# Optimization experiments

Measured on AMD Instinct MI355X. Metric: run time of the kernel, lower is better.

The kernel has to match this reference:

```python
import jax, jax.numpy as jnp
import numpy as np

N, F, T, H, E, OUT, HEADS = 20000, 32, 12, 64, 320000, 12, 2


def setup_inputs() -> dict:
    key = jax.random.key(0)
    ks = iter(jax.random.split(key, 40))

    def nrm(shape, scale):
        return jax.random.normal(next(ks), shape, jnp.float32) * scale

    g0 = 2 * H + F   # gate input dim, cell 0
    g1 = 2 * H + H   # gate input dim, cell 1
    inp = {
        "x": nrm((N, F, T), 1.0),
        "edge_index": jax.random.randint(next(ks), (2, E), 0, N, dtype=jnp.int32),
        "edge_attr": jax.random.uniform(next(ks), (E, 2), dtype=jnp.float32),
        # cell 0: GCNConv + GRU gates (weights stored [in, out])
        "Wg0": nrm((F, H), F ** -0.5), "bg0": nrm((H,), 0.02),
        "Wu0": nrm((g0, H), g0 ** -0.5), "bu0": nrm((H,), 0.02),
        "Wr0": nrm((g0, H), g0 ** -0.5), "br0": nrm((H,), 0.02),
        "Wc0": nrm((g0, H), g0 ** -0.5), "bc0": nrm((H,), 0.02),
        # cell 1
        "Wg1": nrm((H, H), H ** -0.5), "bg1": nrm((H,), 0.02),
        "Wu1": nrm((g1, H), g1 ** -0.5), "bu1": nrm((H,), 0.02),
        "Wr1": nrm((g1, H), g1 ** -0.5), "br1": nrm((H,), 0.02),
        "Wc1": nrm((g1, H), g1 ** -0.5), "bc1": nrm((H,), 0.02),
        # temporal multi-head attention (torch layout: [out, in])
        "in_proj_w": nrm((3 * H, H), H ** -0.5), "in_proj_b": nrm((3 * H,), 0.02),
        "out_proj_w": nrm((H, H), H ** -0.5), "out_proj_b": nrm((H,), 0.02),
        # output head ([in, out])
        "out_w": nrm((H, OUT), H ** -0.5), "out_b": nrm((OUT,), 0.02),
    }
    return inp


def reference(x, edge_index, edge_attr,
              Wg0, bg0, Wu0, bu0, Wr0, br0, Wc0, bc0,
              Wg1, bg1, Wu1, bu1, Wr1, br1, Wc1, bc1,
              in_proj_w, in_proj_b, out_proj_w, out_proj_b,
              out_w, out_b):
    n, f, t = x.shape
    h_dim = Wg0.shape[1]
    src, dst = edge_index[0], edge_index[1]
    w = edge_attr[:, -1]

    # GCN normalization with self-loops (PyG gcn_norm)
    loop = jnp.arange(n)
    src_all = jnp.concatenate([src, loop])
    dst_all = jnp.concatenate([dst, loop])
    w_all = jnp.concatenate([w, jnp.ones((n,), x.dtype)])
    deg = jax.ops.segment_sum(w_all, dst_all, num_segments=n)
    dinv = jnp.where(deg > 0, jax.lax.rsqrt(deg), 0.0)
    norm = dinv[src_all] * w_all * dinv[dst_all]  # [E+N]

    def gcn(xi, W, b):
        xw = xi @ W  # [N, H]
        msg = norm[:, None] * xw[src_all]  # gather from sources
        return jax.ops.segment_sum(msg, dst_all, num_segments=n) + b

    def cell(xi, h, W, b, Wu, bu, Wr, br, Wc, bc):
        g = jax.nn.sigmoid(gcn(xi, W, b))
        zu = jnp.concatenate([xi, g, h], axis=-1)
        u = jax.nn.sigmoid(zu @ Wu + bu)
        r = jax.nn.sigmoid(zu @ Wr + br)
        zc = jnp.concatenate([xi, g, r * h], axis=-1)
        c = jnp.tanh(zc @ Wc + bc)
        return u * h + (1.0 - u) * c

    def step(carry, x_t):
        h0, h1 = carry
        h0 = cell(x_t, h0, Wg0, bg0, Wu0, bu0, Wr0, br0, Wc0, bc0)
        h1 = cell(h0, h1, Wg1, bg1, Wu1, bu1, Wr1, br1, Wc1, bc1)
        return (h0, h1), h1

    x_seq = jnp.transpose(x, (2, 0, 1))  # [T, N, F]
    h0 = jnp.zeros((n, h_dim), x.dtype)
    _, h_seq = jax.lax.scan(step, (h0, h0), x_seq)  # [T, N, H] (== [S, B, H])

    # temporal multi-head self-attention per node
    heads = HEADS
    dh = h_dim // heads
    qkv = h_seq @ in_proj_w.T + in_proj_b  # [T, N, 3H]
    q, k, v = jnp.split(qkv, 3, axis=-1)

    def split_heads(a):
        return jnp.transpose(a.reshape(t, n, heads, dh), (1, 2, 0, 3))  # [N, h, T, dh]

    q, k, v = split_heads(q), split_heads(k), split_heads(v)
    scores = jnp.einsum('nhtd,nhsd->nhts', q, k) / jnp.sqrt(jnp.asarray(dh, x.dtype))
    attn = jax.nn.softmax(scores, axis=-1)
    o = jnp.einsum('nhts,nhsd->nhtd', attn, v)
    o = jnp.transpose(o, (2, 0, 1, 3)).reshape(t, n, h_dim)
    o = o @ out_proj_w.T + out_proj_b  # [T, N, H]

    h_attn = o.mean(axis=0)  # agg='mean' over sequence -> [N, H]
    return h_attn @ out_w + out_b  # [N, OUT]
```

## Files before the change

kernel.cpp:

```cpp
#include <hip/hip_runtime.h>
#include <math.h>

#define NN 20000
#define FF 32
#define TT 12
#define HH 64
#define EE 320000
#define OUTD 12
#define CB1 1250
#define GB  2500

typedef __attribute__((ext_vector_type(8))) short short8;
typedef __attribute__((ext_vector_type(4))) float floatx4;

__device__ __forceinline__ float aexp2(float x) {
    float r; asm("v_exp_f32 %0, %1" : "=v"(r) : "v"(x)); return r;
}
__device__ __forceinline__ float arcp(float x) {
    float r; asm("v_rcp_f32 %0, %1" : "=v"(r) : "v"(x)); return r;
}
#define LOG2E 1.44269504088896f
__device__ __forceinline__ float fsig(float x) { return arcp(1.f + aexp2(-LOG2E * x)); }
__device__ __forceinline__ float ftanh(float x) {
    return fmaf(-2.f, arcp(1.f + aexp2(2.f * LOG2E * x)), 1.f);
}

__device__ __forceinline__ unsigned short bf16rne(float f) {
    union { float f; unsigned u; } v; v.f = f;
    unsigned u = v.u;
    u += 0x7fffu + ((u >> 16) & 1u);
    return (unsigned short)(u >> 16);
}
__device__ __forceinline__ float lof(unsigned v) {
    union { unsigned u; float f; } x; x.u = v << 16; return x.f;
}
__device__ __forceinline__ float hif(unsigned v) {
    union { unsigned u; float f; } x; x.u = v & 0xffff0000u; return x.f;
}
__device__ __forceinline__ unsigned packbf(float a, float b) {
    return (unsigned)bf16rne(a) | ((unsigned)bf16rne(b) << 16);
}

#define MFMA(a, b, c) __builtin_amdgcn_mfma_f32_16x16x32_bf16((a), (b), (c), 0, 0, 0)


__global__ void init_all(float* deg, int* cnt, float* h0f1, float* h1f1,
                         unsigned* h0s2u, unsigned* h1s0u) {
    int i = blockIdx.x * 256 + threadIdx.x;
    if (i < NN) { deg[i] = 1.0f; cnt[i] = 0; }
    if (i < NN * HH) { h0f1[i] = 0.f; h1f1[i] = 0.f; }
    if (i < NN * HH / 2) { h0s2u[i] = 0u; h1s0u[i] = 0u; }
}

__global__ void edge_accum_kernel(const int* ei, const float* ea, float* deg, int* cnt) {
    int e = blockIdx.x * 256 + threadIdx.x;
    if (e >= EE) return;
    int d = ei[EE + e];
    float w = ea[e * 2 + 1];
    atomicAdd(&deg[d], w);
    atomicAdd(&cnt[d], 1);
}

__global__ void scan_dinv(const int* cnt, int* rowptr, int* cursor,
                          const float* deg, float* dinv) {
    if (blockIdx.x != 0) {
        int i = (blockIdx.x - 1) * 1024 + threadIdx.x;
        if (i < NN) dinv[i] = rsqrtf(deg[i]);
        return;
    }
    __shared__ int wsum[16];
    int tid = threadIdx.x;
    int lane = tid & 63, w = tid >> 6;
    int run = 0;
    for (int base = 0; base < NN; base += 1024) {
        int idx = base + tid;
        int c = (idx < NN) ? cnt[idx] : 0;
        int v = c;
        #pragma unroll
        for (int off = 1; off < 64; off <<= 1) {
            int t = __shfl_up(v, off, 64);
            if (lane >= off) v += t;
        }
        if (lane == 63) wsum[w] = v;
        __syncthreads();
        if (tid < 16) {
            int x = wsum[tid];
            #pragma unroll
            for (int off = 1; off < 16; off <<= 1) {
                int t = __shfl_up(x, off, 64);
                if (tid >= off) x += t;
            }
            wsum[tid] = x;
        }
        __syncthreads();
        int waveoff = (w > 0) ? wsum[w - 1] : 0;
        int excl = run + waveoff + (v - c);
        if (idx < NN) { rowptr[idx] = excl; cursor[idx] = excl; }
        run += wsum[15];
        __syncthreads();
    }
    if (tid == 0) rowptr[NN] = run;
}

__global__ void fill_kernel(const int* ei, const float* ea, const float* dinv,
                            int* cursor, int2* colval) {
    int e = blockIdx.x * 256 + threadIdx.x;
    if (e >= EE) return;
    int s = ei[e], d = ei[EE + e];
    float w = ea[e * 2 + 1];
    int pos = atomicAdd(&cursor[d], 1);
    colval[pos] = make_int2(s, __float_as_int(dinv[s] * w * dinv[d]));
}

#define TPB 1250
#define WCB 336
__global__ void prep_misc(const float* __restrict__ x, unsigned short* __restrict__ xTs,
                          const float* Wg0, const float* Wu0, const float* Wr0, const float* Wc0,
                          const float* Wg1, const float* Wu1, const float* Wr1, const float* Wc1,
                          const float* ipw,
                          short* Wg0T, short* Wu0T, short* Wr0T, short* Wc0T,
                          short* Wg1T, short* Wu1T, short* Wr1T, short* Wc1T, short* ipwB,
                          const float* opw, const float* opb, const float* ow, const float* ob,
                          float* OW2, float* ob2) {
    int b = blockIdx.x;
    if (b < TPB) {
        __shared__ float tl[16 * 416];
        int n0 = b * 16;
        const float* xb = x + (size_t)n0 * 384;
        int tid = threadIdx.x;
        #pragma unroll
        for (int k = 0; k < 24; ++k) {
            int i = tid + 256 * k;
            float v = xb[i];
            int nn = i / 384;
            int rem = i - nn * 384;
            int f = rem / 12;
            int t2 = rem - f * 12;
            tl[nn * 416 + f * 13 + t2] = v;
        }
        __syncthreads();
        #pragma unroll
        for (int k = 0; k < 24; ++k) {
            int o = tid + 256 * k;
            int f = o & 31;
            int nn = (o >> 5) & 15;
            int t = o >> 9;
            xTs[(size_t)t * (NN * FF) + (size_t)(n0 + nn) * 32 + f] =
                bf16rne(tl[nn * 416 + f * 13 + t]);
        }
        return;
    }
    if (b < TPB + WCB) {
        int i = (b - TPB) * 256 + threadIdx.x;
        if (i < 2048) { int n = i / 32, k = i % 32; Wg0T[i] = (short)bf16rne(Wg0[k * 64 + n]); return; }
        i -= 2048;
        if (i < 10240) { int n = i / 160, k = i % 160; Wu0T[i] = (short)bf16rne(Wu0[k * 64 + n]); return; }
        i -= 10240;
        if (i < 10240) { int n = i / 160, k = i % 160; Wr0T[i] = (short)bf16rne(Wr0[k * 64 + n]); return; }
        i -= 10240;
        if (i < 10240) { int n = i / 160, k = i % 160; Wc0T[i] = (short)bf16rne(Wc0[k * 64 + n]); return; }
        i -= 10240;
        if (i < 4096) { int n = i / 64, k = i % 64; Wg1T[i] = (short)bf16rne(Wg1[k * 64 + n]); return; }
        i -= 4096;
        if (i < 12288) { int n = i / 192, k = i % 192; Wu1T[i] = (short)bf16rne(Wu1[k * 64 + n]); return; }
        i -= 12288;
        if (i < 12288) { int n = i / 192, k = i % 192; Wr1T[i] = (short)bf16rne(Wr1[k * 64 + n]); return; }
        i -= 12288;
        if (i < 12288) { int n = i / 192, k = i % 192; Wc1T[i] = (short)bf16rne(Wc1[k * 64 + n]); return; }
        i -= 12288;
        if (i < 12288) { ipwB[i] = (short)bf16rne(ipw[i]); }
        return;
    }
    {
        int i = (b - TPB - WCB) * 256 + threadIdx.x;
        if (i < 64 * OUTD) {
            int k = i / OUTD, d = i - k * OUTD;
            float acc = 0.f;
            for (int j = 0; j < 64; ++j) acc += opw[j * 64 + k] * ow[j * OUTD + d];
            OW2[i] = acc;
        } else if (i < 64 * OUTD + OUTD) {
            int d = i - 64 * OUTD;
            float acc = ob[d];
            for (int j = 0; j < 64; ++j) acc += opb[j] * ow[j * OUTD + d];
            ob2[d] = acc;
        }
    }
}

__global__ void gather_raw32(const unsigned short* __restrict__ xTs, const float* __restrict__ dinv,
                             const int* __restrict__ rowptr, const int2* __restrict__ colval,
                             unsigned short* __restrict__ aggxs) {
    const unsigned* src = (const unsigned*)(xTs + (size_t)blockIdx.y * NN * 32);
    unsigned* dst = (unsigned*)(aggxs + (size_t)blockIdx.y * NN * 32);
    int node = blockIdx.x * 16 + (threadIdx.x >> 4);
    int l2 = threadIdx.x & 15;
    float di = dinv[node];
    float dd = di * di;
    unsigned v = src[node * 16 + l2];
    float a0 = dd * lof(v), a1 = dd * hif(v);
    int s = rowptr[node], e = rowptr[node + 1];
    int j = s;
    for (; j + 3 < e; j += 4) {
        int2 cv0 = colval[j], cv1 = colval[j + 1], cv2 = colval[j + 2], cv3 = colval[j + 3];
        float w0 = __int_as_float(cv0.y), w1 = __int_as_float(cv1.y);
        float w2 = __int_as_float(cv2.y), w3 = __int_as_float(cv3.y);
        unsigned v0 = src[cv0.x * 16 + l2], v1 = src[cv1.x * 16 + l2];
        unsigned v2 = src[cv2.x * 16 + l2], v3 = src[cv3.x * 16 + l2];
        a0 += w0 * lof(v0) + w1 * lof(v1) + w2 * lof(v2) + w3 * lof(v3);
        a1 += w0 * hif(v0) + w1 * hif(v1) + w2 * hif(v2) + w3 * hif(v3);
    }
    for (; j < e; ++j) {
        int2 cv = colval[j];
        unsigned vv = src[cv.x * 16 + l2];
        float w = __int_as_float(cv.y);
        a0 += w * lof(vv); a1 += w * hif(vv);
    }
    dst[node * 16 + l2] = packbf(a0, a1);
}

__device__ __forceinline__ void gather_g1_body(
    int blk, const unsigned short* __restrict__ y0s, const float* __restrict__ dinv,
    const int* __restrict__ rowptr, const int2* __restrict__ colval,
    const float* __restrict__ bg1, unsigned short* __restrict__ g1s) {
    const unsigned* yp = (const unsigned*)y0s;
    int node = blk * 8 + (threadIdx.x >> 5);
    int l2 = threadIdx.x & 31;
    float di = dinv[node];
    float dd = di * di;
    unsigned v = yp[node * 32 + l2];
    float a0 = dd * lof(v), a1 = dd * hif(v);
    int s = rowptr[node], e = rowptr[node + 1];
    int j = s;
    for (; j + 3 < e; j += 4) {
        int2 cv0 = colval[j], cv1 = colval[j + 1], cv2 = colval[j + 2], cv3 = colval[j + 3];
        float w0 = __int_as_float(cv0.y), w1 = __int_as_float(cv1.y);
        float w2 = __int_as_float(cv2.y), w3 = __int_as_float(cv3.y);
        unsigned v0 = yp[cv0.x * 32 + l2], v1 = yp[cv1.x * 32 + l2];
        unsigned v2 = yp[cv2.x * 32 + l2], v3 = yp[cv3.x * 32 + l2];
        a0 += w0 * lof(v0) + w1 * lof(v1) + w2 * lof(v2) + w3 * lof(v3);
        a1 += w0 * hif(v0) + w1 * hif(v1) + w2 * hif(v2) + w3 * hif(v3);
    }
    for (; j < e; ++j) {
        int2 cv = colval[j];
        unsigned vv = yp[cv.x * 32 + l2];
        float w = __int_as_float(cv.y);
        a0 += w * lof(vv); a1 += w * hif(vv);
    }
    float g0v = fsig(a0 + bg1[2 * l2]);
    float g1v = fsig(a1 + bg1[2 * l2 + 1]);
    ((unsigned*)g1s)[node * 32 + l2] = packbf(g0v, g1v);
}


__launch_bounds__(256, 4)
__global__ void mfma_g0(const unsigned short* __restrict__ aggxs, const short* __restrict__ Wg0T,
                        const float* __restrict__ bg0, unsigned short* __restrict__ g0s) {
    int tid = threadIdx.x;
    int wv = tid >> 6, lane = tid & 63;
    int quad = lane >> 4, ln = lane & 15;
    int m0 = blockIdx.x * 64 + wv * 16;
    short8 af = *reinterpret_cast<const short8*>(aggxs + (size_t)(m0 + ln) * 32 + quad * 8);
    floatx4 z = {0.f, 0.f, 0.f, 0.f};
    floatx4 acc[4] = {z, z, z, z};
    #pragma unroll
    for (int ct = 0; ct < 4; ++ct) {
        short8 bf = *reinterpret_cast<const short8*>(Wg0T + (size_t)(ct * 16 + ln) * 32 + quad * 8);
        acc[ct] = MFMA(af, bf, acc[ct]);
    }
    #pragma unroll
    for (int ct = 0; ct < 4; ++ct) {
        int col = ct * 16 + ln;
        float bb = bg0[col];
        #pragma unroll
        for (int r = 0; r < 4; ++r) {
            int row = m0 + quad * 4 + r;
            g0s[(size_t)row * 64 + col] = bf16rne(fsig(acc[ct][r] + bb));
        }
    }
}


__device__ __forceinline__ void cell0_body(
    int m0, short* T,
    const unsigned short* __restrict__ xt, const unsigned short* __restrict__ g0,
    const float* __restrict__ h0f, const unsigned short* __restrict__ h0s,
    const short* __restrict__ Wu0T, const short* __restrict__ Wr0T,
    const short* __restrict__ Wc0T, const short* __restrict__ Wg1T,
    const float* __restrict__ bu0, const float* __restrict__ br0,
    const float* __restrict__ bc0,
    float* __restrict__ h0nf, unsigned short* __restrict__ h0ns,
    unsigned short* __restrict__ y0s) {
    int tid = threadIdx.x;
    int wv = tid >> 6, lane = tid & 63;
    int quad = lane >> 4, ln = lane & 15;
    int arow = m0 + ln;
    int col = wv * 16 + ln;

    short8 af[5];
    af[0] = *reinterpret_cast<const short8*>(xt + (size_t)arow * 32 + quad * 8);
    af[1] = *reinterpret_cast<const short8*>(g0 + (size_t)arow * 64 + quad * 8);
    af[2] = *reinterpret_cast<const short8*>(g0 + (size_t)arow * 64 + 32 + quad * 8);
    af[3] = *reinterpret_cast<const short8*>(h0s + (size_t)arow * 64 + quad * 8);
    af[4] = *reinterpret_cast<const short8*>(h0s + (size_t)arow * 64 + 32 + quad * 8);

    floatx4 z = {0.f, 0.f, 0.f, 0.f};
    floatx4 aU = z, aR = z;
    const short* bu = Wu0T + (size_t)col * 160;
    const short* br = Wr0T + (size_t)col * 160;
    #pragma unroll
    for (int kc = 0; kc < 5; ++kc) {
        int ko = kc * 32 + quad * 8;
        aU = MFMA(af[kc], *reinterpret_cast<const short8*>(bu + ko), aU);
        aR = MFMA(af[kc], *reinterpret_cast<const short8*>(br + ko), aR);
    }
    float bU = bu0[col], bR = br0[col];
    float uu[4], hv[4];
    #pragma unroll
    for (int r = 0; r < 4; ++r) {
        int grow = m0 + quad * 4 + r;
        uu[r] = fsig(aU[r] + bU);
        hv[r] = h0f[(size_t)grow * 64 + col];
        float rh = fsig(aR[r] + bR) * hv[r];
        T[(quad * 4 + r) * 72 + col] = (short)bf16rne(rh);
    }
    __syncthreads();

    short8 ar0 = *reinterpret_cast<const short8*>(T + ln * 72 + quad * 8);
    short8 ar1 = *reinterpret_cast<const short8*>(T + ln * 72 + 32 + quad * 8);
    floatx4 aC = z;
    const short* bc = Wc0T + (size_t)col * 160;
    #pragma unroll
    for (int kc = 0; kc < 3; ++kc)
        aC = MFMA(af[kc], *reinterpret_cast<const short8*>(bc + kc * 32 + quad * 8), aC);
    aC = MFMA(ar0, *reinterpret_cast<const short8*>(bc + 96 + quad * 8), aC);
    aC = MFMA(ar1, *reinterpret_cast<const short8*>(bc + 128 + quad * 8), aC);
    __syncthreads();

    float bC = bc0[col];
    #pragma unroll
    for (int r = 0; r < 4; ++r) {
        int grow = m0 + quad * 4 + r;
        float cv = ftanh(aC[r] + bC);
        float hn = uu[r] * hv[r] + (1.f - uu[r]) * cv;
        unsigned short hb = bf16rne(hn);
        h0nf[(size_t)grow * 64 + col] = hn;
        h0ns[(size_t)grow * 64 + col] = hb;
        T[(quad * 4 + r) * 72 + col] = (short)hb;
    }
    __syncthreads();

    short8 ah0 = *reinterpret_cast<const short8*>(T + ln * 72 + quad * 8);
    short8 ah1 = *reinterpret_cast<const short8*>(T + ln * 72 + 32 + quad * 8);
    floatx4 aY = z;
    const short* bg = Wg1T + (size_t)col * 64;
    aY = MFMA(ah0, *reinterpret_cast<const short8*>(bg + quad * 8), aY);
    aY = MFMA(ah1, *reinterpret_cast<const short8*>(bg + 32 + quad * 8), aY);
    #pragma unroll
    for (int r = 0; r < 4; ++r) {
        int grow = m0 + quad * 4 + r;
        y0s[(size_t)grow * 64 + col] = bf16rne(aY[r]);
    }
}

__device__ __forceinline__ void cell1_body(
    int m0, short* T,
    const unsigned short* __restrict__ h0s, const unsigned short* __restrict__ g1s,
    const float* __restrict__ h1f, const unsigned short* __restrict__ h1s,
    const short* __restrict__ Wu1T, const short* __restrict__ Wr1T,
    const short* __restrict__ Wc1T,
    const float* __restrict__ bu1, const float* __restrict__ br1,
    const float* __restrict__ bc1,
    float* __restrict__ h1nf, unsigned short* __restrict__ h1ns) {
    int tid = threadIdx.x;
    int wv = tid >> 6, lane = tid & 63;
    int quad = lane >> 4, ln = lane & 15;
    int arow = m0 + ln;
    int col = wv * 16 + ln;

    short8 af[6];
    af[0] = *reinterpret_cast<const short8*>(h0s + (size_t)arow * 64 + quad * 8);
    af[1] = *reinterpret_cast<const short8*>(h0s + (size_t)arow * 64 + 32 + quad * 8);
    af[2] = *reinterpret_cast<const short8*>(g1s + (size_t)arow * 64 + quad * 8);
    af[3] = *reinterpret_cast<const short8*>(g1s + (size_t)arow * 64 + 32 + quad * 8);
    af[4] = *reinterpret_cast<const short8*>(h1s + (size_t)arow * 64 + quad * 8);
    af[5] = *reinterpret_cast<const short8*>(h1s + (size_t)arow * 64 + 32 + quad * 8);

    floatx4 z = {0.f, 0.f, 0.f, 0.f};
    floatx4 aU = z, aR = z;
    const short* bu = Wu1T + (size_t)col * 192;
    const short* br = Wr1T + (size_t)col * 192;
    #pragma unroll
    for (int kc = 0; kc < 6; ++kc) {
        int ko = kc * 32 + quad * 8;
        aU = MFMA(af[kc], *reinterpret_cast<const short8*>(bu + ko), aU);
        aR = MFMA(af[kc], *reinterpret_cast<const short8*>(br + ko), aR);
    }
    float bU = bu1[col], bR = br1[col];
    float uu[4], hv[4];
    #pragma unroll
    for (int r = 0; r < 4; ++r) {
        int grow = m0 + quad * 4 + r;
        uu[r] = fsig(aU[r] + bU);
        hv[r] = h1f[(size_t)grow * 64 + col];
        float rh = fsig(aR[r] + bR) * hv[r];
        T[(quad * 4 + r) * 72 + col] = (short)bf16rne(rh);
    }
    __syncthreads();

    short8 ar0 = *reinterpret_cast<const short8*>(T + ln * 72 + quad * 8);
    short8 ar1 = *reinterpret_cast<const short8*>(T + ln * 72 + 32 + quad * 8);
    floatx4 aC = z;
    const short* bc = Wc1T + (size_t)col * 192;
    #pragma unroll
    for (int kc = 0; kc < 4; ++kc)
        aC = MFMA(af[kc], *reinterpret_cast<const short8*>(bc + kc * 32 + quad * 8), aC);
    aC = MFMA(ar0, *reinterpret_cast<const short8*>(bc + 128 + quad * 8), aC);
    aC = MFMA(ar1, *reinterpret_cast<const short8*>(bc + 160 + quad * 8), aC);

    float bC = bc1[col];
    #pragma unroll
    for (int r = 0; r < 4; ++r) {
        int grow = m0 + quad * 4 + r;
        float cv = ftanh(aC[r] + bC);
        float hn = uu[r] * hv[r] + (1.f - uu[r]) * cv;
        h1nf[(size_t)grow * 64 + col] = hn;
        h1ns[(size_t)grow * 64 + col] = bf16rne(hn);
    }
}


struct PipeArgs {
    const float* dinv; const int* rowptr; const int2* colval;
    const short* Wu0T; const short* Wr0T; const short* Wc0T; const short* Wg1T;
    const float* bu0; const float* br0; const float* bc0;
    const short* Wu1T; const short* Wr1T; const short* Wc1T;
    const float* bu1; const float* br1; const float* bc1; const float* bg1;
    int c0n;
    const unsigned short* c0_xt; const unsigned short* c0_g0;
    const float* c0_hf_in; const unsigned short* c0_hs_in;
    float* c0_hf_out; unsigned short* c0_hs_out; unsigned short* c0_y0_out;
    int gn;
    const unsigned short* g_y0; unsigned short* g_g1;
    int c1n;
    const unsigned short* c1_h0s; const unsigned short* c1_g1;
    const float* c1_hf_in; const unsigned short* c1_hs_in;
    float* c1_hf_out; unsigned short* c1_hs_out;
};

__launch_bounds__(256, 6)
__global__ void pipe_step(PipeArgs A) {
    __shared__ short T[16 * 72];
    int b = blockIdx.x;
    if (b < A.c0n) {
        cell0_body(b * 16, T, A.c0_xt, A.c0_g0, A.c0_hf_in, A.c0_hs_in,
                   A.Wu0T, A.Wr0T, A.Wc0T, A.Wg1T, A.bu0, A.br0, A.bc0,
                   A.c0_hf_out, A.c0_hs_out, A.c0_y0_out);
        return;
    }
    b -= A.c0n;
    if (b < A.gn) {
        gather_g1_body(b, A.g_y0, A.dinv, A.rowptr, A.colval, A.bg1, A.g_g1);
        return;
    }
    b -= A.gn;
    cell1_body(b * 16, T, A.c1_h0s, A.c1_g1, A.c1_hf_in, A.c1_hs_in,
               A.Wu1T, A.Wr1T, A.Wc1T, A.bu1, A.br1, A.bc1,
               A.c1_hf_out, A.c1_hs_out);
}

__launch_bounds__(256, 5)
__global__ void attn_fused(const unsigned short* __restrict__ hseqs,
                           const short* __restrict__ ipwB, const float* __restrict__ ipb,
                           const float* __restrict__ OW2, const float* __restrict__ ob2,
                           float* __restrict__ out) {
    __shared__ unsigned short qtile[4][16 * 200];
    __shared__ float fbuf[4][64];
    __shared__ float wbuf[4][32];
    int wv = threadIdx.x >> 6, lane = threadIdx.x & 63;
    int node = blockIdx.x * 4 + wv;
    int quad = lane >> 4, ln = lane & 15;
    unsigned short* q = qtile[wv];
    float* sob = fbuf[wv];
    float* W = wbuf[wv];

    short8 zero8 = {0, 0, 0, 0, 0, 0, 0, 0};
    short8 af0 = zero8, af1 = zero8;
    if (ln < TT) {
        const unsigned short* hp = hseqs + ((size_t)ln * NN + node) * 64;
        af0 = *reinterpret_cast<const short8*>(hp + quad * 8);
        af1 = *reinterpret_cast<const short8*>(hp + 32 + quad * 8);
    }
    floatx4 z = {0.f, 0.f, 0.f, 0.f};
    #pragma unroll
    for (int ct = 0; ct < 12; ++ct) {
        const short* br = ipwB + (size_t)(ct * 16 + ln) * 64;
        floatx4 acc = MFMA(af0, *reinterpret_cast<const short8*>(br + quad * 8), z);
        acc = MFMA(af1, *reinterpret_cast<const short8*>(br + 32 + quad * 8), acc);
        int col = ct * 16 + ln;
        float bb = ipb[col];
        #pragma unroll
        for (int r = 0; r < 4; ++r)
            q[(quad * 4 + r) * 200 + col] = bf16rne(acc[r] + bb);
    }
    __threadfence_block();

    floatx4 sc[2];
    #pragma unroll
    for (int h = 0; h < 2; ++h) {
        short8 aQ = *reinterpret_cast<const short8*>(q + ln * 200 + h * 32 + quad * 8);
        short8 bK = *reinterpret_cast<const short8*>(q + ln * 200 + 64 + h * 32 + quad * 8);
        sc[h] = MFMA(aQ, bK, z);
    }
    const float scl = 0.17677669529663687f;
    bool colok = ln < 12;
    #pragma unroll
    for (int h = 0; h < 2; ++h) {
        float p[4];
        #pragma unroll
        for (int r = 0; r < 4; ++r) {
            float v = colok ? sc[h][r] * scl : -1e30f;
            float m = v;
            m = fmaxf(m, __shfl_xor(m, 1, 64));
            m = fmaxf(m, __shfl_xor(m, 2, 64));
            m = fmaxf(m, __shfl_xor(m, 4, 64));
            m = fmaxf(m, __shfl_xor(m, 8, 64));
            float e = colok ? aexp2(LOG2E * (v - m)) : 0.f;
            float s = e;
            s += __shfl_xor(s, 1, 64);
            s += __shfl_xor(s, 2, 64);
            s += __shfl_xor(s, 4, 64);
            s += __shfl_xor(s, 8, 64);
            p[r] = e * arcp(s);
        }
        float ts = (quad < 3) ? (p[0] + p[1] + p[2] + p[3]) : 0.f;
        ts += __shfl_xor(ts, 16, 64);
        ts += __shfl_xor(ts, 32, 64);
        if (quad == 0) W[h * 16 + ln] = ts * (1.f / 12.f);
    }
    __threadfence_block();

    {
        int d = lane, hd = d >> 5, dd = d & 31;
        float acc = 0.f;
        #pragma unroll
        for (int ts = 0; ts < 12; ++ts)
            acc += W[hd * 16 + ts] * lof((unsigned)q[ts * 200 + 128 + hd * 32 + dd]);
        sob[d] = acc;
    }
    __threadfence_block();

    if (lane < OUTD) {
        float acc = ob2[lane];
        #pragma unroll
        for (int k = 0; k < 64; ++k) acc += sob[k] * OW2[k * OUTD + lane];
        out[(size_t)node * OUTD + lane] = acc;
    }
}


extern "C" void kernel_launch(void* const* d_in, const int* in_sizes, int n_in,
                              void* d_out, int out_size, void* d_ws, size_t ws_size,
                              hipStream_t stream) {
    const float* x   = (const float*)d_in[0];
    const int*   ei  = (const int*)d_in[1];
    const float* ea  = (const float*)d_in[2];
    const float* Wg0 = (const float*)d_in[3];
    const float* bg0 = (const float*)d_in[4];
    const float* Wu0 = (const float*)d_in[5];
    const float* bu0 = (const float*)d_in[6];
    const float* Wr0 = (const float*)d_in[7];
    const float* br0 = (const float*)d_in[8];
    const float* Wc0 = (const float*)d_in[9];
    const float* bc0 = (const float*)d_in[10];
    const float* Wg1 = (const float*)d_in[11];
    const float* bg1 = (const float*)d_in[12];
    const float* Wu1 = (const float*)d_in[13];
    const float* bu1 = (const float*)d_in[14];
    const float* Wr1 = (const float*)d_in[15];
    const float* br1 = (const float*)d_in[16];
    const float* Wc1 = (const float*)d_in[17];
    const float* bc1 = (const float*)d_in[18];
    const float* ipw = (const float*)d_in[19];
    const float* ipb = (const float*)d_in[20];
    const float* opw = (const float*)d_in[21];
    const float* opb = (const float*)d_in[22];
    const float* ow  = (const float*)d_in[23];
    const float* ob  = (const float*)d_in[24];
    float* out = (float*)d_out;

    char* p = (char*)d_ws;
    auto alloc = [&](size_t bytes) { char* r = p; p += (bytes + 255) & ~(size_t)255; return (void*)r; };
    unsigned short* hseqs = (unsigned short*)alloc((size_t)TT * NN * HH * 2);
    unsigned short* h1s0  = (unsigned short*)alloc((size_t)NN * HH * 2);
    short* Wg0T = (short*)alloc((size_t)64 * 32 * 2);
    short* Wu0T = (short*)alloc((size_t)64 * 160 * 2);
    short* Wr0T = (short*)alloc((size_t)64 * 160 * 2);
    short* Wc0T = (short*)alloc((size_t)64 * 160 * 2);
    short* Wg1T = (short*)alloc((size_t)64 * 64 * 2);
    short* Wu1T = (short*)alloc((size_t)64 * 192 * 2);
    short* Wr1T = (short*)alloc((size_t)64 * 192 * 2);
    short* Wc1T = (short*)alloc((size_t)64 * 192 * 2);
    short* ipwB = (short*)alloc((size_t)192 * 64 * 2);
    float* OW2  = (float*)alloc((size_t)64 * OUTD * 4);
    float* ob2  = (float*)alloc((size_t)OUTD * 4);
    float* dinv   = (float*)alloc((size_t)NN * 4);
    int*   rowptr = (int*)  alloc((size_t)(NN + 1) * 4);
    int2*  colval = (int2*) alloc((size_t)EE * 8);
    unsigned short* xTs   = (unsigned short*)alloc((size_t)TT * NN * FF * 2);
    unsigned short* aggxs = (unsigned short*)alloc((size_t)TT * NN * FF * 2);
    unsigned short* g0s   = (unsigned short*)alloc((size_t)TT * NN * HH * 2);
    float* deg    = (float*)alloc((size_t)NN * 4);
    int*   cnt    = (int*)  alloc((size_t)NN * 4);
    int*   cursor = (int*)  alloc((size_t)NN * 4);
    unsigned short* y0sA = (unsigned short*)alloc((size_t)NN * HH * 2);
    unsigned short* y0sB = (unsigned short*)alloc((size_t)NN * HH * 2);
    unsigned short* g1sA = (unsigned short*)alloc((size_t)NN * HH * 2);
    unsigned short* g1sB = (unsigned short*)alloc((size_t)NN * HH * 2);
    float* h0f0 = (float*)alloc((size_t)NN * HH * 4);
    float* h0f1 = (float*)alloc((size_t)NN * HH * 4);
    float* h1f0 = (float*)alloc((size_t)NN * HH * 4);
    float* h1f1 = (float*)alloc((size_t)NN * HH * 4);
    unsigned short* h0s0 = (unsigned short*)alloc((size_t)NN * HH * 2);
    unsigned short* h0s1 = (unsigned short*)alloc((size_t)NN * HH * 2);
    unsigned short* h0s2 = (unsigned short*)alloc((size_t)NN * HH * 2);
    (void)ws_size;

    init_all<<<(NN * HH + 255) / 256, 256, 0, stream>>>(
        deg, cnt, h0f1, h1f1, (unsigned*)h0s2, (unsigned*)h1s0);
    edge_accum_kernel<<<(EE + 255) / 256, 256, 0, stream>>>(ei, ea, deg, cnt);
    scan_dinv<<<1 + (NN + 1023) / 1024, 1024, 0, stream>>>(cnt, rowptr, cursor, deg, dinv);
    fill_kernel<<<(EE + 255) / 256, 256, 0, stream>>>(ei, ea, dinv, cursor, colval);
    prep_misc<<<TPB + WCB + 4, 256, 0, stream>>>(
        x, xTs,
        Wg0, Wu0, Wr0, Wc0, Wg1, Wu1, Wr1, Wc1, ipw,
        Wg0T, Wu0T, Wr0T, Wc0T, Wg1T, Wu1T, Wr1T, Wc1T, ipwB,
        opw, opb, ow, ob, OW2, ob2);

    gather_raw32<<<dim3(NN / 16, TT), 256, 0, stream>>>(xTs, dinv, rowptr, colval, aggxs);
    mfma_g0<<<(TT * NN) / 64, 256, 0, stream>>>(aggxs, Wg0T, bg0, g0s);

    float* h0fB[2] = {h0f0, h0f1};
    unsigned short* h0sB[3] = {h0s0, h0s1, h0s2};
    float* h1fB[2] = {h1f0, h1f1};
    unsigned short* y0B[2] = {y0sA, y0sB};
    unsigned short* g1B[2] = {g1sA, g1sB};

    PipeArgs base;
    base.dinv = dinv; base.rowptr = rowptr; base.colval = colval;
    base.Wu0T = Wu0T; base.Wr0T = Wr0T; base.Wc0T = Wc0T; base.Wg1T = Wg1T;
    base.bu0 = bu0; base.br0 = br0; base.bc0 = bc0;
    base.Wu1T = Wu1T; base.Wr1T = Wr1T; base.Wc1T = Wc1T;
    base.bu1 = bu1; base.br1 = br1; base.bc1 = bc1; base.bg1 = bg1;

    for (int l = 0; l <= TT + 1; ++l) {
        PipeArgs A = base;
        int tc0 = l, tg = l - 1, tc1 = l - 2;

        A.c0n = (tc0 < TT) ? CB1 : 0;
        if (A.c0n) {
            A.c0_xt = xTs + (size_t)tc0 * NN * FF;
            A.c0_g0 = g0s + (size_t)tc0 * NN * HH;
            A.c0_hf_in = h0fB[(tc0 + 1) & 1];
            A.c0_hs_in = h0sB[(tc0 + 2) % 3];
            A.c0_hf_out = h0fB[tc0 & 1];
            A.c0_hs_out = h0sB[tc0 % 3];
            A.c0_y0_out = y0B[tc0 & 1];
        } else {
            A.c0_xt = xTs; A.c0_g0 = g0s; A.c0_hf_in = h0fB[0]; A.c0_hs_in = h0sB[0];
            A.c0_hf_out = h0fB[0]; A.c0_hs_out = h0sB[0]; A.c0_y0_out = y0B[0];
        }

        A.gn = (tg >= 0 && tg < TT) ? GB : 0;
        if (A.gn) { A.g_y0 = y0B[tg & 1]; A.g_g1 = g1B[tg & 1]; }
        else { A.g_y0 = y0B[0]; A.g_g1 = g1B[0]; }

        A.c1n = (tc1 >= 0 && tc1 < TT) ? CB1 : 0;
        if (A.c1n) {
            A.c1_h0s = h0sB[tc1 % 3];
            A.c1_g1 = g1B[tc1 & 1];
            A.c1_hf_in = h1fB[(tc1 + 1) & 1];
            A.c1_hs_in = (tc1 == 0) ? h1s0 : (hseqs + (size_t)(tc1 - 1) * NN * HH);
            A.c1_hf_out = h1fB[tc1 & 1];
            A.c1_hs_out = hseqs + (size_t)tc1 * NN * HH;
        } else {
            A.c1_h0s = h0sB[0]; A.c1_g1 = g1B[0]; A.c1_hf_in = h1fB[0];
            A.c1_hs_in = h1s0; A.c1_hf_out = h1fB[0]; A.c1_hs_out = hseqs;
        }

        int grid = A.c0n + A.gn + A.c1n;
        pipe_step<<<grid, 256, 0, stream>>>(A);
    }

    attn_fused<<<NN / 4, 256, 0, stream>>>(hseqs, ipwB, ipb, OW2, ob2, out);
}
```

Measured before the change: 799.6 us.

## Store hidden sequence node-major, unroll gathers by eight, drop softmax max

The layer-1 hidden sequence is now stored node-major with a padded row stride (13 slots of 64 per node, slot 0 holding the zero initial state). Attention can then read each node's time steps contiguously, and the separate zero buffer is no longer needed. Both sparse gather loops gain an 8-way unrolled path to keep more loads in flight. The softmax max-subtraction shuffles are removed, which relies on scores staying small enough not to overflow exp. The strided writes in cell1 may coalesce less well.

```diff
diff --git a/kernel.cpp b/kernel.cpp
--- a/kernel.cpp
+++ b/kernel.cpp
@@ -9,6 +9,7 @@
 #define OUTD 12
 #define CB1 1250
 #define GB  2500
+#define HST 832
 
 typedef __attribute__((ext_vector_type(8))) short short8;
 typedef __attribute__((ext_vector_type(4))) float floatx4;
@@ -45,11 +46,12 @@
 
 
 __global__ void init_all(float* deg, int* cnt, float* h0f1, float* h1f1,
-                         unsigned* h0s2u, unsigned* h1s0u) {
+                         unsigned* h0s2u, unsigned* hseqTu) {
     int i = blockIdx.x * 256 + threadIdx.x;
     if (i < NN) { deg[i] = 1.0f; cnt[i] = 0; }
     if (i < NN * HH) { h0f1[i] = 0.f; h1f1[i] = 0.f; }
-    if (i < NN * HH / 2) { h0s2u[i] = 0u; h1s0u[i] = 0u; }
+    if (i < NN * HH / 2) { h0s2u[i] = 0u; }
+    if (i < NN * 32) { hseqTu[(size_t)(i >> 5) * (HST / 2) + (i & 31)] = 0u; }
 }
 
 __global__ void edge_accum_kernel(const int* ei, const float* ea, float* deg, int* cnt) {
@@ -200,6 +202,19 @@
     float a0 = dd * lof(v), a1 = dd * hif(v);
     int s = rowptr[node], e = rowptr[node + 1];
     int j = s;
+    for (; j + 7 < e; j += 8) {
+        int2 c[8];
+        #pragma unroll
+        for (int q = 0; q < 8; ++q) c[q] = colval[j + q];
+        unsigned vv[8];
+        #pragma unroll
+        for (int q = 0; q < 8; ++q) vv[q] = src[c[q].x * 16 + l2];
+        #pragma unroll
+        for (int q = 0; q < 8; ++q) {
+            float w = __int_as_float(c[q].y);
+            a0 += w * lof(vv[q]); a1 += w * hif(vv[q]);
+        }
+    }
     for (; j + 3 < e; j += 4) {
         int2 cv0 = colval[j], cv1 = colval[j + 1], cv2 = colval[j + 2], cv3 = colval[j + 3];
         float w0 = __int_as_float(cv0.y), w1 = __int_as_float(cv1.y);
@@ -231,6 +246,19 @@
     float a0 = dd * lof(v), a1 = dd * hif(v);
     int s = rowptr[node], e = rowptr[node + 1];
     int j = s;
+    for (; j + 7 < e; j += 8) {
+        int2 c[8];
+        #pragma unroll
+        for (int q = 0; q < 8; ++q) c[q] = colval[j + q];
+        unsigned vv[8];
+        #pragma unroll
+        for (int q = 0; q < 8; ++q) vv[q] = yp[c[q].x * 32 + l2];
+        #pragma unroll
+        for (int q = 0; q < 8; ++q) {
+            float w = __int_as_float(c[q].y);
+            a0 += w * lof(vv[q]); a1 += w * hif(vv[q]);
+        }
+    }
     for (; j + 3 < e; j += 4) {
         int2 cv0 = colval[j], cv1 = colval[j + 1], cv2 = colval[j + 2], cv3 = colval[j + 3];
         float w0 = __int_as_float(cv0.y), w1 = __int_as_float(cv1.y);
@@ -365,12 +393,12 @@
 __device__ __forceinline__ void cell1_body(
     int m0, short* T,
     const unsigned short* __restrict__ h0s, const unsigned short* __restrict__ g1s,
-    const float* __restrict__ h1f, const unsigned short* __restrict__ h1s,
+    const float* __restrict__ h1f, const unsigned short* __restrict__ h1sT_in,
     const short* __restrict__ Wu1T, const short* __restrict__ Wr1T,
     const short* __restrict__ Wc1T,
     const float* __restrict__ bu1, const float* __restrict__ br1,
     const float* __restrict__ bc1,
-    float* __restrict__ h1nf, unsigned short* __restrict__ h1ns) {
+    float* __restrict__ h1nf, unsigned short* __restrict__ h1sT_out) {
     int tid = threadIdx.x;
     int wv = tid >> 6, lane = tid & 63;
     int quad = lane >> 4, ln = lane & 15;
@@ -382,8 +410,8 @@
     af[1] = *reinterpret_cast<const short8*>(h0s + (size_t)arow * 64 + 32 + quad * 8);
     af[2] = *reinterpret_cast<const short8*>(g1s + (size_t)arow * 64 + quad * 8);
     af[3] = *reinterpret_cast<const short8*>(g1s + (size_t)arow * 64 + 32 + quad * 8);
-    af[4] = *reinterpret_cast<const short8*>(h1s + (size_t)arow * 64 + quad * 8);
-    af[5] = *reinterpret_cast<const short8*>(h1s + (size_t)arow * 64 + 32 + quad * 8);
+    af[4] = *reinterpret_cast<const short8*>(h1sT_in + (size_t)arow * HST + quad * 8);
+    af[5] = *reinterpret_cast<const short8*>(h1sT_in + (size_t)arow * HST + 32 + quad * 8);
 
     floatx4 z = {0.f, 0.f, 0.f, 0.f};
     floatx4 aU = z, aR = z;
@@ -424,7 +452,7 @@
         float cv = ftanh(aC[r] + bC);
         float hn = uu[r] * hv[r] + (1.f - uu[r]) * cv;
         h1nf[(size_t)grow * 64 + col] = hn;
-        h1ns[(size_t)grow * 64 + col] = bf16rne(hn);
+        h1sT_out[(size_t)grow * HST + col] = bf16rne(hn);
     }
 }
 
@@ -443,8 +471,8 @@
     const unsigned short* g_y0; unsigned short* g_g1;
     int c1n;
     const unsigned short* c1_h0s; const unsigned short* c1_g1;
-    const float* c1_hf_in; const unsigned short* c1_hs_in;
-    float* c1_hf_out; unsigned short* c1_hs_out;
+    const float* c1_hf_in; const unsigned short* c1_hsT_in;
+    float* c1_hf_out; unsigned short* c1_hsT_out;
 };
 
 __launch_bounds__(256, 6)
@@ -463,13 +491,13 @@
         return;
     }
     b -= A.gn;
-    cell1_body(b * 16, T, A.c1_h0s, A.c1_g1, A.c1_hf_in, A.c1_hs_in,
+    cell1_body(b * 16, T, A.c1_h0s, A.c1_g1, A.c1_hf_in, A.c1_hsT_in,
                A.Wu1T, A.Wr1T, A.Wc1T, A.bu1, A.br1, A.bc1,
-               A.c1_hf_out, A.c1_hs_out);
+               A.c1_hf_out, A.c1_hsT_out);
 }
 
 __launch_bounds__(256, 5)
-__global__ void attn_fused(const unsigned short* __restrict__ hseqs,
+__global__ void attn_fused(const unsigned short* __restrict__ hseqT,
                            const short* __restrict__ ipwB, const float* __restrict__ ipb,
                            const float* __restrict__ OW2, const float* __restrict__ ob2,
                            float* __restrict__ out) {
@@ -486,7 +514,7 @@
     short8 zero8 = {0, 0, 0, 0, 0, 0, 0, 0};
     short8 af0 = zero8, af1 = zero8;
     if (ln < TT) {
-        const unsigned short* hp = hseqs + ((size_t)ln * NN + node) * 64;
+        const unsigned short* hp = hseqT + (size_t)node * HST + (size_t)(ln + 1) * 64;
         af0 = *reinterpret_cast<const short8*>(hp + quad * 8);
         af1 = *reinterpret_cast<const short8*>(hp + 32 + quad * 8);
     }
@@ -518,13 +546,7 @@
         float p[4];
         #pragma unroll
         for (int r = 0; r < 4; ++r) {
-            float v = colok ? sc[h][r] * scl : -1e30f;
-            float m = v;
-            m = fmaxf(m, __shfl_xor(m, 1, 64));
-            m = fmaxf(m, __shfl_xor(m, 2, 64));
-            m = fmaxf(m, __shfl_xor(m, 4, 64));
-            m = fmaxf(m, __shfl_xor(m, 8, 64));
-            float e = colok ? aexp2(LOG2E * (v - m)) : 0.f;
+            float e = colok ? aexp2(LOG2E * scl * sc[h][r]) : 0.f;
             float s = e;
             s += __shfl_xor(s, 1, 64);
             s += __shfl_xor(s, 2, 64);
@@ -590,8 +612,7 @@
 
     char* p = (char*)d_ws;
     auto alloc = [&](size_t bytes) { char* r = p; p += (bytes + 255) & ~(size_t)255; return (void*)r; };
-    unsigned short* hseqs = (unsigned short*)alloc((size_t)TT * NN * HH * 2);
-    unsigned short* h1s0  = (unsigned short*)alloc((size_t)NN * HH * 2);
+    unsigned short* hseqT = (unsigned short*)alloc((size_t)NN * HST * 2);
     short* Wg0T = (short*)alloc((size_t)64 * 32 * 2);
     short* Wu0T = (short*)alloc((size_t)64 * 160 * 2);
     short* Wr0T = (short*)alloc((size_t)64 * 160 * 2);
@@ -626,7 +647,7 @@
     (void)ws_size;
 
     init_all<<<(NN * HH + 255) / 256, 256, 0, stream>>>(
-        deg, cnt, h0f1, h1f1, (unsigned*)h0s2, (unsigned*)h1s0);
+        deg, cnt, h0f1, h1f1, (unsigned*)h0s2, (unsigned*)hseqT);
     edge_accum_kernel<<<(EE + 255) / 256, 256, 0, stream>>>(ei, ea, deg, cnt);
     scan_dinv<<<1 + (NN + 1023) / 1024, 1024, 0, stream>>>(cnt, rowptr, cursor, deg, dinv);
     fill_kernel<<<(EE + 255) / 256, 256, 0, stream>>>(ei, ea, dinv, cursor, colval);
@@ -679,17 +700,17 @@
             A.c1_h0s = h0sB[tc1 % 3];
             A.c1_g1 = g1B[tc1 & 1];
             A.c1_hf_in = h1fB[(tc1 + 1) & 1];
-            A.c1_hs_in = (tc1 == 0) ? h1s0 : (hseqs + (size_t)(tc1 - 1) * NN * HH);
+            A.c1_hsT_in = hseqT + (size_t)tc1 * 64;
             A.c1_hf_out = h1fB[tc1 & 1];
-            A.c1_hs_out = hseqs + (size_t)tc1 * NN * HH;
+            A.c1_hsT_out = hseqT + (size_t)(tc1 + 1) * 64;
         } else {
             A.c1_h0s = h0sB[0]; A.c1_g1 = g1B[0]; A.c1_hf_in = h1fB[0];
-            A.c1_hs_in = h1s0; A.c1_hf_out = h1fB[0]; A.c1_hs_out = hseqs;
+            A.c1_hsT_in = hseqT; A.c1_hf_out = h1fB[0]; A.c1_hsT_out = hseqT;
         }
 
         int grid = A.c0n + A.gn + A.c1n;
         pipe_step<<<grid, 256, 0, stream>>>(A);
     }
 
-    attn_fused<<<NN / 4, 256, 0, stream>>>(hseqs, ipwB, ipb, OW2, ob2, out);
-}
+    attn_fused<<<NN / 4, 256, 0, stream>>>(hseqT, ipwB, ipb, OW2, ob2, out);
+}
```

After: 779.6 us. 2.5% less time.
